# Performance work log

Measured on AMD Instinct MI355X. Metric: run time of the kernel, lower is better.

Reference implementation:

```python
import jax, jax.numpy as jnp
import numpy as np

T, N, D, B, L = 4, 1_000_000, 4, 16_384, 50
TOTAL = B * L

def setup_inputs() -> dict:
    key = jax.random.key(0)
    k0, k1, k2, k3, k4 = jax.random.split(key, 5)
    tables = jax.random.normal(k0, (T, N, D), dtype=jnp.float32) * 0.01
    indices = jax.random.randint(k1, (T, TOTAL), 0, N)
    # sorted segment ids encode jagged bag boundaries (variable lengths per sample)
    segment_ids = jnp.sort(jax.random.randint(k2, (T, TOTAL), 0, B), axis=-1)
    W = jax.random.normal(k3, (1, D), dtype=jnp.float32) * (1.0 / np.sqrt(D))
    b = jax.random.normal(k4, (1,), dtype=jnp.float32) * 0.01
    return {"tables": tables, "W": W, "b": b, "indices": indices, "segment_ids": segment_ids}

def reference(tables, W, b, indices, segment_ids):
    # EmbeddingBagCollection: per-table gather + sum pooling over jagged bags
    def pool_one(tbl, idx, seg):
        rows = tbl[idx]                                   # [TOTAL, D] irregular gather
        return jax.ops.segment_sum(rows, seg, num_segments=B)  # [B, D]
    pooled = jax.vmap(pool_one)(tables, indices, segment_ids)  # [T, B, D]
    # to_dict() + per-key append + cat(dim=0)  ==  reshape stacking tables along batch
    sparse_features = pooled.reshape(T * B, D)            # [T*B, D]
    # over_arch Linear(4, 1)
    return sparse_features @ W.T + b                      # [T*B, 1]
```

## Files before the change

kernel.cpp:

```cpp
#include <hip/hip_runtime.h>

constexpr int T     = 4;
constexpr int NROWS = 1000000;
constexpr int B     = 16384;
constexpr int TOTAL = 16384 * 50;

typedef float fv4 __attribute__((ext_vector_type(4)));
typedef int   iv2 __attribute__((ext_vector_type(2)));


__global__ __launch_bounds__(256)
void produce_kernel(const fv4*   __restrict__ tables,
                    const float* __restrict__ Wp,
                    const float* __restrict__ bias,
                    float* __restrict__ p,
                    float* __restrict__ out) {
    const int i = blockIdx.x * 256 + threadIdx.x;
    if (i < T * NROWS) {
        const float wx = Wp[0], wy = Wp[1], wz = Wp[2], ww = Wp[3];
        const fv4 r = tables[i];
        p[i] = r.x * wx + r.y * wy + r.z * wz + r.w * ww;
    }
    if (i < T * B) out[i] = bias[0];
}

__global__ __launch_bounds__(256)
void pool_kernel(const float* __restrict__ p,
                 const iv2*   __restrict__ indices,
                 const iv2*   __restrict__ segids,
                 float*       __restrict__ out)
{
    const int xcd    = blockIdx.x & 7;
    const int t      = xcd >> 1;
    const int within = ((blockIdx.x >> 3) << 1) + (xcd & 1);
    const int q      = within * 256 + threadIdx.x;
    const int gq     = t * (TOTAL / 2) + q;
    const int lane   = threadIdx.x & 63;

    const iv2 s2 = __builtin_nontemporal_load(&segids[gq]);
    const iv2 i2 = __builtin_nontemporal_load(&indices[gq]);

    const float* pt = p + t * NROWS;
    const float v0 = pt[i2.x];
    const float v1 = pt[i2.y];

    const int s0 = s2.x, s1 = s2.y;

    const float a0 = v0;
    const float a1 = v1 + (s1 == s0 ? v0 : 0.f);

    float x   = a1;
    int   key = s1;
    #pragma unroll
    for (int d = 1; d < 64; d <<= 1) {
        const float ov = __shfl_up(x, d, 64);
        const int   ok = __shfl_up(key, d, 64);
        if (lane >= d && ok == key) x += ov;
    }

    const float xprev = __shfl_up(x, 1, 64);
    const int   kprev = __shfl_up(key, 1, 64);
    const float carry = (lane > 0 && kprev == s0) ? xprev : 0.f;

    float* outt = out + t * B;
    if (s0 != s1) atomicAdd(&outt[s0], a0 + carry);

    const int snext = __shfl_down(s0, 1, 64);
    if (lane == 63 || snext != key) atomicAdd(&outt[key], x);
}

extern "C" void kernel_launch(void* const* d_in, const int* in_sizes, int n_in,
                              void* d_out, int out_size, void* d_ws, size_t ws_size,
                              hipStream_t stream) {
    const fv4*   tables  = (const fv4*)d_in[0];
    const float* W       = (const float*)d_in[1];
    const float* bias    = (const float*)d_in[2];
    const iv2*   indices = (const iv2*)d_in[3];
    const iv2*   segids  = (const iv2*)d_in[4];
    float*       out     = (float*)d_out;

    float* p = (float*)d_ws;

    {
        int n = T * NROWS;
        produce_kernel<<<(n + 255) / 256, 256, 0, stream>>>(tables, W, bias, p, out);
    }
    {
        pool_kernel<<<6400, 256, 0, stream>>>(p, indices, segids, out);
    }
}
```

Baseline: 133.6 us.

## Fuse projection and pooling into one cooperative kernel with grid sync

Replaces the two launches (row projection, then gather-pool) with a single cooperative persistent kernel of 2048 blocks. Each block first projects its share of table rows, then waits on a grid-wide barrier and runs the same segmented-scan pooling over strided chunks. Blocks are mapped to XCDs per table so that each table's projected rows are written and later read by the same XCD pair, which may improve L2 locality. This saves one launch and the gap between kernels, at the cost of a grid barrier, persistent-loop overhead and possibly lower occupancy; if the cooperative launch fails it falls back to the old two kernels.

```diff
diff --git a/kernel.cpp b/kernel.cpp
--- a/kernel.cpp
+++ b/kernel.cpp
@@ -1,13 +1,92 @@
 #include <hip/hip_runtime.h>
+#include <hip/hip_cooperative_groups.h>
+
+namespace cg = cooperative_groups;
 
 constexpr int T     = 4;
 constexpr int NROWS = 1000000;
 constexpr int B     = 16384;
 constexpr int TOTAL = 16384 * 50;
 
+constexpr int NBLK        = 2048;
+constexpr int BLKS_PER_T  = NBLK / T;
+constexpr int ROW_CHUNKS  = (NROWS + 255) / 256;
+constexpr int PAIR_CHUNKS = (TOTAL / 2) / 256;
+
 typedef float fv4 __attribute__((ext_vector_type(4)));
 typedef int   iv2 __attribute__((ext_vector_type(2)));
 
+
+__global__ __launch_bounds__(256, 8)
+void fused_kernel(const fv4*   __restrict__ tables,
+                  const float* __restrict__ Wp,
+                  const float* __restrict__ bias,
+                  const iv2*   __restrict__ indices,
+                  const iv2*   __restrict__ segids,
+                  float*       __restrict__ p,
+                  float*       __restrict__ out)
+{
+    const int xcd = blockIdx.x & 7;
+    const int t   = xcd >> 1;
+    const int w   = ((blockIdx.x >> 3) << 1) + (xcd & 1);
+    const int tid = threadIdx.x;
+
+    const float wx = Wp[0], wy = Wp[1], wz = Wp[2], ww = Wp[3];
+
+    {
+        const int flat = blockIdx.x * 256 + tid;
+        if (flat < T * B) out[flat] = bias[0];
+    }
+
+    const fv4* tbl = tables + t * NROWS;
+    float*     pt  = p      + t * NROWS;
+    for (int c = w; c < ROW_CHUNKS; c += BLKS_PER_T) {
+        const int r = c * 256 + tid;
+        if (r < NROWS) {
+            const fv4 row = tbl[r];
+            pt[r] = row.x * wx + row.y * wy + row.z * wz + row.w * ww;
+        }
+    }
+
+    cg::this_grid().sync();
+
+    const iv2*  idx_t = indices + t * (TOTAL / 2);
+    const iv2*  seg_t = segids  + t * (TOTAL / 2);
+    float*      outt  = out + t * B;
+    const int   lane  = tid & 63;
+
+    for (int c = w; c < PAIR_CHUNKS; c += BLKS_PER_T) {
+        const int q = c * 256 + tid;
+
+        const iv2 s2 = __builtin_nontemporal_load(&seg_t[q]);
+        const iv2 i2 = __builtin_nontemporal_load(&idx_t[q]);
+
+        const float v0 = pt[i2.x];
+        const float v1 = pt[i2.y];
+        const int   s0 = s2.x, s1 = s2.y;
+
+        const float a0 = v0;
+        const float a1 = v1 + (s1 == s0 ? v0 : 0.f);
+
+        float x   = a1;
+        int   key = s1;
+        #pragma unroll
+        for (int d = 1; d < 64; d <<= 1) {
+            const float ov = __shfl_up(x, d, 64);
+            const int   ok = __shfl_up(key, d, 64);
+            if (lane >= d && ok == key) x += ov;
+        }
+
+        const float xprev = __shfl_up(x, 1, 64);
+        const int   kprev = __shfl_up(key, 1, 64);
+        const float carry = (lane > 0 && kprev == s0) ? xprev : 0.f;
+
+        if (s0 != s1) atomicAdd(&outt[s0], a0 + carry);
+
+        const int snext = __shfl_down(s0, 1, 64);
+        if (lane == 63 || snext != key) atomicAdd(&outt[key], x);
+    }
+}
 
 __global__ __launch_bounds__(256)
 void produce_kernel(const fv4*   __restrict__ tables,
@@ -28,8 +107,7 @@
 void pool_kernel(const float* __restrict__ p,
                  const iv2*   __restrict__ indices,
                  const iv2*   __restrict__ segids,
-                 float*       __restrict__ out)
-{
+                 float*       __restrict__ out) {
     const int xcd    = blockIdx.x & 7;
     const int t      = xcd >> 1;
     const int within = ((blockIdx.x >> 3) << 1) + (xcd & 1);
@@ -43,7 +121,6 @@
     const float* pt = p + t * NROWS;
     const float v0 = pt[i2.x];
     const float v1 = pt[i2.y];
-
     const int s0 = s2.x, s1 = s2.y;
 
     const float a0 = v0;
@@ -64,7 +141,6 @@
 
     float* outt = out + t * B;
     if (s0 != s1) atomicAdd(&outt[s0], a0 + carry);
-
     const int snext = __shfl_down(s0, 1, 64);
     if (lane == 63 || snext != key) atomicAdd(&outt[key], x);
 }
@@ -81,11 +157,15 @@
 
     float* p = (float*)d_ws;
 
-    {
+    void* args[] = { (void*)&tables, (void*)&W, (void*)&bias,
+                     (void*)&indices, (void*)&segids, (void*)&p, (void*)&out };
+    hipError_t err = hipLaunchCooperativeKernel((const void*)fused_kernel,
+                                                dim3(NBLK), dim3(256),
+                                                args, 0, stream);
+    if (err != hipSuccess) {
+        (void)hipGetLastError();
         int n = T * NROWS;
         produce_kernel<<<(n + 255) / 256, 256, 0, stream>>>(tables, W, bias, p, out);
-    }
-    {
         pool_kernel<<<6400, 256, 0, stream>>>(p, indices, segids, out);
     }
 }
```

Result: slower. 292.7 us (+119.2%).
